# Kernel optimization log

Measured on AMD Instinct MI355X. Metric: run time of the kernel, lower is better.

Reference implementation:

```python
import jax, jax.numpy as jnp
import numpy as np


def quat_to_rot(q):
    # q: [B,4] as (w, x, y, z); normalize then standard quaternion->rotation.
    q = q / jnp.linalg.norm(q, axis=-1, keepdims=True)
    w, x, y, z = q[:, 0], q[:, 1], q[:, 2], q[:, 3]
    R = jnp.stack([
        jnp.stack([1 - 2 * (y * y + z * z), 2 * (x * y - w * z), 2 * (x * z + w * y)], axis=-1),
        jnp.stack([2 * (x * y + w * z), 1 - 2 * (x * x + z * z), 2 * (y * z - w * x)], axis=-1),
        jnp.stack([2 * (x * z - w * y), 2 * (y * z + w * x), 1 - 2 * (x * x + y * y)], axis=-1),
    ], axis=-2)  # [B,3,3]
    return R


def setup_inputs() -> dict:
    key = jax.random.key(0)
    k1, k2, k3, k4 = jax.random.split(key, 4)
    B, N = 16, 500000
    return {
        "pcd_mis": jax.random.normal(k1, (B, N, 3), dtype=jnp.float32),
        "T_mis": jax.random.normal(k2, (B, 4, 4), dtype=jnp.float32),
        "delta_q_pred": jax.random.normal(k3, (B, 4), dtype=jnp.float32),
        "delta_t_pred": jax.random.normal(k4, (B, 3), dtype=jnp.float32),
    }


def reference(pcd_mis, T_mis, delta_q_pred, delta_t_pred):
    B = delta_q_pred.shape[0]
    R = quat_to_rot(delta_q_pred)                       # [B,3,3]
    t = delta_t_pred[:, :, None]                        # [B,3,1]
    top = jnp.concatenate([R, t], axis=-1)              # [B,3,4]
    bottom = jnp.broadcast_to(jnp.array([0.0, 0.0, 0.0, 1.0], dtype=top.dtype), (B, 1, 4))
    delta_T = jnp.concatenate([top, bottom], axis=-2)   # [B,4,4]
    delta_T_inv = jnp.linalg.inv(delta_T)               # [B,4,4]
    batch_T_pred = jnp.einsum('bij,bjk->bik', delta_T_inv, T_mis)  # [B,4,4]
    # rigid transform of point clouds: p' = R_inv p + t_inv
    R_inv = delta_T_inv[:, :3, :3]
    t_inv = delta_T_inv[:, :3, 3]
    pcd_realigned = jnp.einsum('bij,bnj->bni', R_inv, pcd_mis) + t_inv[:, None, :]
    return (batch_T_pred, pcd_realigned)
```

## Files before the change

kernel.cpp:

```cpp
#include <hip/hip_runtime.h>

__device__ __forceinline__ void inv_rigid(const float* __restrict__ dq,
                                          const float* __restrict__ dt,
                                          int b,
                                          float& i00, float& i01, float& i02,
                                          float& i10, float& i11, float& i12,
                                          float& i20, float& i21, float& i22,
                                          float& tix, float& tiy, float& tiz) {
    float qw = dq[b * 4 + 0];
    float qx = dq[b * 4 + 1];
    float qy = dq[b * 4 + 2];
    float qz = dq[b * 4 + 3];
    float inv = 1.0f / sqrtf(qw * qw + qx * qx + qy * qy + qz * qz);
    qw *= inv; qx *= inv; qy *= inv; qz *= inv;

    float r00 = 1.0f - 2.0f * (qy * qy + qz * qz);
    float r01 = 2.0f * (qx * qy - qw * qz);
    float r02 = 2.0f * (qx * qz + qw * qy);
    float r10 = 2.0f * (qx * qy + qw * qz);
    float r11 = 1.0f - 2.0f * (qx * qx + qz * qz);
    float r12 = 2.0f * (qy * qz - qw * qx);
    float r20 = 2.0f * (qx * qz - qw * qy);
    float r21 = 2.0f * (qy * qz + qw * qx);
    float r22 = 1.0f - 2.0f * (qx * qx + qy * qy);

    i00 = r00; i01 = r10; i02 = r20;
    i10 = r01; i11 = r11; i12 = r21;
    i20 = r02; i21 = r12; i22 = r22;

    float tx = dt[b * 3 + 0];
    float ty = dt[b * 3 + 1];
    float tz = dt[b * 3 + 2];
    tix = -(i00 * tx + i01 * ty + i02 * tz);
    tiy = -(i10 * tx + i11 * ty + i12 * tz);
    tiz = -(i20 * tx + i21 * ty + i22 * tz);
}

__global__ void batch_T_kernel(const float* __restrict__ T_mis,
                               const float* __restrict__ dq,
                               const float* __restrict__ dt,
                               float* __restrict__ out_T,
                               int B) {
    int b = threadIdx.x;
    if (b >= B) return;

    float i00, i01, i02, i10, i11, i12, i20, i21, i22, tix, tiy, tiz;
    inv_rigid(dq, dt, b, i00, i01, i02, i10, i11, i12, i20, i21, i22, tix, tiy, tiz);

    const float* T = T_mis + b * 16;
    float* O = out_T + b * 16;

    float Ri[3][3] = {{i00, i01, i02}, {i10, i11, i12}, {i20, i21, i22}};
    float ti[3] = {tix, tiy, tiz};
#pragma unroll
    for (int i = 0; i < 3; ++i) {
#pragma unroll
        for (int k = 0; k < 4; ++k) {
            O[i * 4 + k] = Ri[i][0] * T[0 * 4 + k] + Ri[i][1] * T[1 * 4 + k] +
                           Ri[i][2] * T[2 * 4 + k] + ti[i] * T[3 * 4 + k];
        }
    }
#pragma unroll
    for (int k = 0; k < 4; ++k) O[3 * 4 + k] = T[3 * 4 + k];
}

__global__ void pcd_kernel(const float4* __restrict__ pin,
                           float4* __restrict__ pout,
                           const float* __restrict__ dq,
                           const float* __restrict__ dt,
                           int groups_per_batch,
                           int rem_points,
                           long long n_per_batch)
{
    int b = blockIdx.y;

    float i00, i01, i02, i10, i11, i12, i20, i21, i22, tix, tiy, tiz;
    inv_rigid(dq, dt, b, i00, i01, i02, i10, i11, i12, i20, i21, i22, tix, tiy, tiz);

    long long base4 = (long long)b * (n_per_batch * 3LL) / 4LL;

    for (long long g = (long long)blockIdx.x * blockDim.x + threadIdx.x;
         g < groups_per_batch;
         g += (long long)gridDim.x * blockDim.x) {
        long long idx = base4 + g * 3LL;
        float4 A = pin[idx];
        float4 Bv = pin[idx + 1];
        float4 C = pin[idx + 2];

        float x0 = A.x, y0 = A.y, z0 = A.z;
        float x1 = A.w, y1 = Bv.x, z1 = Bv.y;
        float x2 = Bv.z, y2 = Bv.w, z2 = C.x;
        float x3 = C.y, y3 = C.z, z3 = C.w;

        float ox0 = i00 * x0 + i01 * y0 + i02 * z0 + tix;
        float oy0 = i10 * x0 + i11 * y0 + i12 * z0 + tiy;
        float oz0 = i20 * x0 + i21 * y0 + i22 * z0 + tiz;

        float ox1 = i00 * x1 + i01 * y1 + i02 * z1 + tix;
        float oy1 = i10 * x1 + i11 * y1 + i12 * z1 + tiy;
        float oz1 = i20 * x1 + i21 * y1 + i22 * z1 + tiz;

        float ox2 = i00 * x2 + i01 * y2 + i02 * z2 + tix;
        float oy2 = i10 * x2 + i11 * y2 + i12 * z2 + tiy;
        float oz2 = i20 * x2 + i21 * y2 + i22 * z2 + tiz;

        float ox3 = i00 * x3 + i01 * y3 + i02 * z3 + tix;
        float oy3 = i10 * x3 + i11 * y3 + i12 * z3 + tiy;
        float oz3 = i20 * x3 + i21 * y3 + i22 * z3 + tiz;

        float4 OA = make_float4(ox0, oy0, oz0, ox1);
        float4 OB = make_float4(oy1, oz1, ox2, oy2);
        float4 OC = make_float4(oz2, ox3, oy3, oz3);
        pout[idx] = OA;
        pout[idx + 1] = OB;
        pout[idx + 2] = OC;
    }

    if (rem_points > 0 && blockIdx.x == 0 && threadIdx.x < (unsigned)rem_points) {
        long long p = (long long)groups_per_batch * 4LL + threadIdx.x;
        const float* fin = (const float*)pin;
        float* fout = (float*)pout;
        long long fbase = (long long)b * (n_per_batch * 3LL) + p * 3LL;
        float x = fin[fbase + 0], y = fin[fbase + 1], z = fin[fbase + 2];
        fout[fbase + 0] = i00 * x + i01 * y + i02 * z + tix;
        fout[fbase + 1] = i10 * x + i11 * y + i12 * z + tiy;
        fout[fbase + 2] = i20 * x + i21 * y + i22 * z + tiz;
    }
}

extern "C" void kernel_launch(void* const* d_in, const int* in_sizes, int n_in,
                              void* d_out, int out_size, void* d_ws, size_t ws_size,
                              hipStream_t stream) {
    const float* pcd = (const float*)d_in[0];
    const float* T_mis = (const float*)d_in[1];
    const float* dq = (const float*)d_in[2];
    const float* dt = (const float*)d_in[3];

    int B = in_sizes[2] / 4;
    long long N = (long long)in_sizes[0] / (3LL * B);

    float* out_T = (float*)d_out;
    float* out_pcd = (float*)d_out + (long long)B * 16;

    batch_T_kernel<<<dim3(1), dim3(64), 0, stream>>>(T_mis, dq, dt, out_T, B);

    int groups = (int)(N / 4);
    int rem = (int)(N % 4);
    int blocks_x = (int)((groups + 255) / 256);
    if (blocks_x < 1) blocks_x = 1;
    dim3 grid(blocks_x, B);
    pcd_kernel<<<grid, dim3(256), 0, stream>>>(
        (const float4*)pcd, (float4*)out_pcd, dq, dt, groups, rem, N);
}
```

Measured before the change: 41.40 us.

## Fuse batch_T into point kernel and use one float4 per thread with shuffles

Computes the 4x4 batch transform inside the point-cloud kernel, so the separate batch_T launch goes away when the per-batch float count is divisible by four. Each thread now loads one float4 instead of three, and fetches the neighbouring coordinates it needs from adjacent lanes with shuffles, using extra global loads at wavefront edges. This gives fully coalesced single-vector accesses and removes a kernel launch. The cost is cross-lane shuffles, divergent branches on m%3, and a scalar fallback path for unaligned sizes.

```diff
diff --git a/kernel.cpp b/kernel.cpp
--- a/kernel.cpp
+++ b/kernel.cpp
@@ -36,96 +36,114 @@
     tiz = -(i20 * tx + i21 * ty + i22 * tz);
 }
 
-__global__ void batch_T_kernel(const float* __restrict__ T_mis,
+__global__ void realign_kernel(const float4* __restrict__ pin,
+                               float4* __restrict__ pout,
+                               const float* __restrict__ T_mis,
                                const float* __restrict__ dq,
                                const float* __restrict__ dt,
                                float* __restrict__ out_T,
-                               int B) {
-    int b = threadIdx.x;
-    if (b >= B) return;
-
-    float i00, i01, i02, i10, i11, i12, i20, i21, i22, tix, tiy, tiz;
-    inv_rigid(dq, dt, b, i00, i01, i02, i10, i11, i12, i20, i21, i22, tix, tiy, tiz);
-
-    const float* T = T_mis + b * 16;
-    float* O = out_T + b * 16;
-
-    float Ri[3][3] = {{i00, i01, i02}, {i10, i11, i12}, {i20, i21, i22}};
-    float ti[3] = {tix, tiy, tiz};
-#pragma unroll
-    for (int i = 0; i < 3; ++i) {
-#pragma unroll
-        for (int k = 0; k < 4; ++k) {
-            O[i * 4 + k] = Ri[i][0] * T[0 * 4 + k] + Ri[i][1] * T[1 * 4 + k] +
-                           Ri[i][2] * T[2 * 4 + k] + ti[i] * T[3 * 4 + k];
-        }
-    }
-#pragma unroll
-    for (int k = 0; k < 4; ++k) O[3 * 4 + k] = T[3 * 4 + k];
-}
-
-__global__ void pcd_kernel(const float4* __restrict__ pin,
-                           float4* __restrict__ pout,
-                           const float* __restrict__ dq,
-                           const float* __restrict__ dt,
-                           int groups_per_batch,
-                           int rem_points,
-                           long long n_per_batch)
+                               int m4_per_batch)
 {
     int b = blockIdx.y;
 
     float i00, i01, i02, i10, i11, i12, i20, i21, i22, tix, tiy, tiz;
     inv_rigid(dq, dt, b, i00, i01, i02, i10, i11, i12, i20, i21, i22, tix, tiy, tiz);
 
-    long long base4 = (long long)b * (n_per_batch * 3LL) / 4LL;
-
-    for (long long g = (long long)blockIdx.x * blockDim.x + threadIdx.x;
-         g < groups_per_batch;
-         g += (long long)gridDim.x * blockDim.x) {
-        long long idx = base4 + g * 3LL;
-        float4 A = pin[idx];
-        float4 Bv = pin[idx + 1];
-        float4 C = pin[idx + 2];
-
-        float x0 = A.x, y0 = A.y, z0 = A.z;
-        float x1 = A.w, y1 = Bv.x, z1 = Bv.y;
-        float x2 = Bv.z, y2 = Bv.w, z2 = C.x;
-        float x3 = C.y, y3 = C.z, z3 = C.w;
-
-        float ox0 = i00 * x0 + i01 * y0 + i02 * z0 + tix;
-        float oy0 = i10 * x0 + i11 * y0 + i12 * z0 + tiy;
-        float oz0 = i20 * x0 + i21 * y0 + i22 * z0 + tiz;
-
-        float ox1 = i00 * x1 + i01 * y1 + i02 * z1 + tix;
-        float oy1 = i10 * x1 + i11 * y1 + i12 * z1 + tiy;
-        float oz1 = i20 * x1 + i21 * y1 + i22 * z1 + tiz;
-
-        float ox2 = i00 * x2 + i01 * y2 + i02 * z2 + tix;
-        float oy2 = i10 * x2 + i11 * y2 + i12 * z2 + tiy;
-        float oz2 = i20 * x2 + i21 * y2 + i22 * z2 + tiz;
-
-        float ox3 = i00 * x3 + i01 * y3 + i02 * z3 + tix;
-        float oy3 = i10 * x3 + i11 * y3 + i12 * z3 + tiy;
-        float oz3 = i20 * x3 + i21 * y3 + i22 * z3 + tiz;
-
-        float4 OA = make_float4(ox0, oy0, oz0, ox1);
-        float4 OB = make_float4(oy1, oz1, ox2, oy2);
-        float4 OC = make_float4(oz2, ox3, oy3, oz3);
-        pout[idx] = OA;
-        pout[idx + 1] = OB;
-        pout[idx + 2] = OC;
+    if (blockIdx.x == 0 && threadIdx.x < 16) {
+        int i = threadIdx.x >> 2, k = threadIdx.x & 3;
+        const float* T = T_mis + b * 16;
+        float val;
+        if (i == 0)      val = i00 * T[k] + i01 * T[4 + k] + i02 * T[8 + k] + tix * T[12 + k];
+        else if (i == 1) val = i10 * T[k] + i11 * T[4 + k] + i12 * T[8 + k] + tiy * T[12 + k];
+        else if (i == 2) val = i20 * T[k] + i21 * T[4 + k] + i22 * T[8 + k] + tiz * T[12 + k];
+        else             val = T[12 + k];
+        out_T[b * 16 + threadIdx.x] = val;
     }
 
-    if (rem_points > 0 && blockIdx.x == 0 && threadIdx.x < (unsigned)rem_points) {
-        long long p = (long long)groups_per_batch * 4LL + threadIdx.x;
-        const float* fin = (const float*)pin;
-        float* fout = (float*)pout;
-        long long fbase = (long long)b * (n_per_batch * 3LL) + p * 3LL;
-        float x = fin[fbase + 0], y = fin[fbase + 1], z = fin[fbase + 2];
-        fout[fbase + 0] = i00 * x + i01 * y + i02 * z + tix;
-        fout[fbase + 1] = i10 * x + i11 * y + i12 * z + tiy;
-        fout[fbase + 2] = i20 * x + i21 * y + i22 * z + tiz;
+    int m = blockIdx.x * blockDim.x + threadIdx.x;
+    long long base = (long long)b * m4_per_batch;
+    bool active = (m < m4_per_batch);
+
+    float4 v = active ? pin[base + m] : make_float4(0.f, 0.f, 0.f, 0.f);
+
+    int lane = threadIdx.x & 63;
+    int r = m % 3;
+
+    float sz = __shfl_up(v.z, 1);
+    float sw = __shfl_up(v.w, 1);
+    float sx = __shfl_down(v.x, 1);
+    float sy = __shfl_down(v.y, 1);
+
+    if (active && lane == 0 && r != 0) {
+        float2 t2 = *(const float2*)((const float*)(pin + base + m - 1) + 2);
+        sz = t2.x; sw = t2.y;
     }
+    if (active && lane == 63 && r != 2) {
+        float2 t2 = *(const float2*)((const float*)(pin + base + m + 1));
+        sx = t2.x; sy = t2.y;
+    }
+
+    float4 o;
+    if (r == 0) {
+        o.x = i00 * v.x + i01 * v.y + i02 * v.z + tix;
+        o.y = i10 * v.x + i11 * v.y + i12 * v.z + tiy;
+        o.z = i20 * v.x + i21 * v.y + i22 * v.z + tiz;
+        o.w = i00 * v.w + i01 * sx  + i02 * sy  + tix;
+    } else if (r == 1) {
+        o.x = i10 * sw  + i11 * v.x + i12 * v.y + tiy;
+        o.y = i20 * sw  + i21 * v.x + i22 * v.y + tiz;
+        o.z = i00 * v.z + i01 * v.w + i02 * sx  + tix;
+        o.w = i10 * v.z + i11 * v.w + i12 * sx  + tiy;
+    } else {
+        o.x = i20 * sz  + i21 * sw  + i22 * v.x + tiz;
+        o.y = i00 * v.y + i01 * v.z + i02 * v.w + tix;
+        o.z = i10 * v.y + i11 * v.z + i12 * v.w + tiy;
+        o.w = i20 * v.y + i21 * v.z + i22 * v.w + tiz;
+    }
+
+    if (active) pout[base + m] = o;
+}
+
+__global__ void realign_scalar_kernel(const float* __restrict__ pin,
+                                      float* __restrict__ pout,
+                                      const float* __restrict__ dq,
+                                      const float* __restrict__ dt,
+                                      long long n_per_batch) {
+    int b = blockIdx.y;
+    float i00, i01, i02, i10, i11, i12, i20, i21, i22, tix, tiy, tiz;
+    inv_rigid(dq, dt, b, i00, i01, i02, i10, i11, i12, i20, i21, i22, tix, tiy, tiz);
+    long long base = (long long)b * n_per_batch * 3LL;
+    for (long long p = (long long)blockIdx.x * blockDim.x + threadIdx.x;
+         p < n_per_batch; p += (long long)gridDim.x * blockDim.x) {
+        float x = pin[base + p * 3 + 0];
+        float y = pin[base + p * 3 + 1];
+        float z = pin[base + p * 3 + 2];
+        pout[base + p * 3 + 0] = i00 * x + i01 * y + i02 * z + tix;
+        pout[base + p * 3 + 1] = i10 * x + i11 * y + i12 * z + tiy;
+        pout[base + p * 3 + 2] = i20 * x + i21 * y + i22 * z + tiz;
+    }
+}
+
+__global__ void batch_T_kernel(const float* __restrict__ T_mis,
+                               const float* __restrict__ dq,
+                               const float* __restrict__ dt,
+                               float* __restrict__ out_T, int B) {
+    int b = threadIdx.x;
+    if (b >= B) return;
+    float i00, i01, i02, i10, i11, i12, i20, i21, i22, tix, tiy, tiz;
+    inv_rigid(dq, dt, b, i00, i01, i02, i10, i11, i12, i20, i21, i22, tix, tiy, tiz);
+    const float* T = T_mis + b * 16;
+    float* O = out_T + b * 16;
+    float Ri[3][3] = {{i00, i01, i02}, {i10, i11, i12}, {i20, i21, i22}};
+    float ti[3] = {tix, tiy, tiz};
+#pragma unroll
+    for (int i = 0; i < 3; ++i)
+#pragma unroll
+        for (int k = 0; k < 4; ++k)
+            O[i * 4 + k] = Ri[i][0] * T[k] + Ri[i][1] * T[4 + k] +
+                           Ri[i][2] * T[8 + k] + ti[i] * T[12 + k];
+#pragma unroll
+    for (int k = 0; k < 4; ++k) O[12 + k] = T[12 + k];
 }
 
 extern "C" void kernel_launch(void* const* d_in, const int* in_sizes, int n_in,
@@ -138,17 +156,23 @@
 
     int B = in_sizes[2] / 4;
     long long N = (long long)in_sizes[0] / (3LL * B);
+    long long nf = N * 3LL;
 
     float* out_T = (float*)d_out;
     float* out_pcd = (float*)d_out + (long long)B * 16;
 
-    batch_T_kernel<<<dim3(1), dim3(64), 0, stream>>>(T_mis, dq, dt, out_T, B);
-
-    int groups = (int)(N / 4);
-    int rem = (int)(N % 4);
-    int blocks_x = (int)((groups + 255) / 256);
-    if (blocks_x < 1) blocks_x = 1;
-    dim3 grid(blocks_x, B);
-    pcd_kernel<<<grid, dim3(256), 0, stream>>>(
-        (const float4*)pcd, (float4*)out_pcd, dq, dt, groups, rem, N);
+    if ((nf & 3LL) == 0LL) {
+        int m4 = (int)(nf >> 2);
+        int blocks_x = (m4 + 255) / 256;
+        dim3 grid(blocks_x, B);
+        realign_kernel<<<grid, dim3(256), 0, stream>>>(
+            (const float4*)pcd, (float4*)out_pcd, T_mis, dq, dt, out_T, m4);
+    } else {
+        batch_T_kernel<<<dim3(1), dim3(64), 0, stream>>>(T_mis, dq, dt, out_T, B);
+        int blocks_x = (int)((N + 255) / 256);
+        if (blocks_x > 4096) blocks_x = 4096;
+        dim3 grid(blocks_x, B);
+        realign_scalar_kernel<<<grid, dim3(256), 0, stream>>>(
+            pcd, out_pcd, dq, dt, N);
+    }
 }
```

After: 39.75 us. 1.04x faster.
